# Kernel optimization log

Hardware: AMD Instinct MI355X
Metric: run time of the kernel (lower is better)

The kernel has to match this reference:

```python
import jax, jax.numpy as jnp
import numpy as np

EL = 512
B = 64
MASK_RAD = 20.0
EPS_SOFT = 0.25  # soft_equality epsilon


def soft_equality(x, value, epsilon):
    return jnp.exp(-((x - value) ** 2) / (2.0 * epsilon ** 2))


def two_point_autocorr(imgs):
    # imgs: (B, el, el). H=2 phases, but iA=iB=0 so only phase 0 contributes.
    el = imgs.shape[-1]
    mf0 = soft_equality(imgs, 0.0, EPS_SOFT)                 # (B, el, el)
    F = jnp.fft.fftn(mf0, axes=(-2, -1))                     # batched 2D FFT
    # term1*term2 = |F| e^{-i ang} * |F| e^{+i ang} = |F|^2 (iA == iB == 0)
    power = (F.real ** 2 + F.imag ** 2) / (el * el)
    ac = jnp.fft.ifftn(power.astype(jnp.complex64), axes=(-2, -1)).real
    # fft_shift: circular roll by half the image in both spatial dims
    return jnp.roll(ac, (el // 2, el // 2), axis=(-2, -1))


def batch_normalize(x):
    # per-image min-max normalization over all pixels
    b = x.shape[0]
    flat = x.reshape(b, -1)
    mn = jnp.min(flat, axis=1, keepdims=True)
    mx = jnp.max(flat, axis=1, keepdims=True)
    out = (flat - mn) / (mx - mn + 1e-12)
    return out.reshape(x.shape)


def gaussian_mask(rad, size):
    y = jnp.arange(size, dtype=jnp.float32)[:, None]
    x = jnp.arange(size, dtype=jnp.float32)[None, :]
    c = size // 2
    d2 = (x - c) ** 2 + (y - c) ** 2
    return jnp.exp(-d2 / (2.0 * rad ** 2))


def setup_inputs() -> dict:
    key = jax.random.key(0)
    k1, k2 = jax.random.split(key)
    inp = jax.random.uniform(k1, (B, 1, EL, EL), dtype=jnp.float32)
    tgt = jax.random.uniform(k2, (B, 1, EL, EL), dtype=jnp.float32)
    return {"input": inp, "target": tgt}


def reference(input, target):
    mask = gaussian_mask(MASK_RAD, EL)  # filtered=True
    ia = batch_normalize(two_point_autocorr(input[:, 0]))[:, None]   # (B,1,el,el)
    ta = batch_normalize(two_point_autocorr(target[:, 0]))[:, None]
    ia = ia * mask
    ta = ta * mask
    diff = jnp.mean((ia - ta) ** 2)
    input_and_ac = jnp.concatenate([input, ia], axis=3)
    target_and_ac = jnp.concatenate([target, ta], axis=3)
    return diff, input_and_ac, target_and_ac
```

## Files before the change

### kernel.cpp

```cpp
#include <hip/hip_runtime.h>

#define EL 512
#define NB 64
#define IMG (EL*EL)
#define HC 256

__device__ __forceinline__ void sb(){ __builtin_amdgcn_sched_barrier(0); }

__device__ __forceinline__ float2 cadd(float2 a, float2 b){ return make_float2(a.x+b.x, a.y+b.y); }
__device__ __forceinline__ float2 csub(float2 a, float2 b){ return make_float2(a.x-b.x, a.y-b.y); }
__device__ __forceinline__ float2 cmul(float2 a, float2 b){ return make_float2(a.x*b.x - a.y*b.y, a.x*b.y + a.y*b.x); }

template<int SIGN> __device__ __forceinline__ float2 mulW4(float2 a);
template<> __device__ __forceinline__ float2 mulW4<-1>(float2 a){ return make_float2( a.y, -a.x); }
template<> __device__ __forceinline__ float2 mulW4< 1>(float2 a){ return make_float2(-a.y,  a.x); }

template<int SIGN>
__device__ __forceinline__ void dft8(const float2* x, float2* X){
  float2 s04=cadd(x[0],x[4]), d04=csub(x[0],x[4]);
  float2 s26=cadd(x[2],x[6]), d26=csub(x[2],x[6]);
  float2 s15=cadd(x[1],x[5]), d15=csub(x[1],x[5]);
  float2 s37=cadd(x[3],x[7]), d37=csub(x[3],x[7]);
  float2 wd26 = mulW4<SIGN>(d26);
  float2 wd37 = mulW4<SIGN>(d37);
  float2 E0=cadd(s04,s26), E2=csub(s04,s26), E1=cadd(d04,wd26), E3=csub(d04,wd26);
  float2 O0=cadd(s15,s37), O2=csub(s15,s37), O1=cadd(d15,wd37), O3=csub(d15,wd37);
  const float C=0.70710678118654752440f;
  float2 w1 = make_float2(C, SIGN*C);
  float2 w3 = make_float2(-C, SIGN*C);
  float2 a1 = cmul(w1, O1);
  float2 a2 = mulW4<SIGN>(O2);
  float2 a3 = cmul(w3, O3);
  X[0]=cadd(E0,O0); X[4]=csub(E0,O0);
  X[1]=cadd(E1,a1); X[5]=csub(E1,a1);
  X[2]=cadd(E2,a2); X[6]=csub(E2,a2);
  X[3]=cadd(E3,a3); X[7]=csub(E3,a3);
}

__device__ __forceinline__ void twiddle8(float2 y[8], float cs, float sn){
  float2 w1 = make_float2(cs, sn);
  float2 w2 = cmul(w1, w1);
  float2 w3 = cmul(w2, w1);
  float2 w4 = cmul(w2, w2);
  float2 w5 = cmul(w4, w1);
  float2 w6 = cmul(w4, w2);
  float2 w7 = cmul(w4, w3);
  y[1] = cmul(y[1], w1);
  y[2] = cmul(y[2], w2);
  y[3] = cmul(y[3], w3);
  y[4] = cmul(y[4], w4);
  y[5] = cmul(y[5], w5);
  y[6] = cmul(y[6], w6);
  y[7] = cmul(y[7], w7);
}

template<int SIGN>
__device__ void fft512(float2 v[8], float2* buf, int lane){
  const float SGN = (float)SIGN;
  float sn, cs;
  float2 y[8];
  dft8<SIGN>(v, y);
  __sincosf(SGN * 0.012271846303085130f * (float)lane, &sn, &cs);
  twiddle8(y, cs, sn);
  sb();
  #pragma unroll
  for (int r=0;r<8;++r) buf[72*r + lane] = y[r];
  sb();
  int k0 = lane >> 3, n0 = lane & 7;
  float2 g[8];
  #pragma unroll
  for (int n1=0;n1<8;++n1) g[n1] = buf[72*k0 + 8*n1 + n0];
  float2 h[8];
  dft8<SIGN>(g, h);
  __sincosf(SGN * 0.098174770424681039f * (float)n0, &sn, &cs);
  twiddle8(h, cs, sn);
  sb();
  #pragma unroll
  for (int r=0;r<8;++r) buf[72*n0 + 9*k0 + r] = h[r];
  sb();
  int k0r = lane & 7, k1r = lane >> 3;
  float2 g2[8];
  #pragma unroll
  for (int m=0;m<8;++m) g2[m] = buf[72*m + 9*k0r + k1r];
  dft8<SIGN>(g2, v);
}

__device__ __forceinline__ unsigned fenc(float f){
  unsigned u = __float_as_uint(f);
  return (u & 0x80000000u) ? ~u : (u | 0x80000000u);
}
__device__ __forceinline__ float fdec(unsigned e){
  return (e & 0x80000000u) ? __uint_as_float(e & 0x7FFFFFFFu) : __uint_as_float(~e);
}

__global__ void k_init(double* accum, unsigned* umin, unsigned* umax){
  int t = threadIdx.x;
  if (t == 0) *accum = 0.0;
  if (t < 2*NB){ umin[t] = 0xFFFFFFFFu; umax[t] = 0u; }
}

__global__ __launch_bounds__(256)
void k_row_fwd(const float* __restrict__ in0, const float* __restrict__ in1,
               float2* __restrict__ cplx, float* __restrict__ outp,
               int base, int Pc){
  __shared__ float2 xbuf[4][576];
  int wave = threadIdx.x >> 6, lane = threadIdx.x & 63;
  int g = blockIdx.x >> 4;
  int rowblk = blockIdx.x & 15;
  bool isin = (g < Pc);
  int b = base + (isin ? g : g - Pc);
  const float* src = (isin ? in0 : in1) + (size_t)b * IMG;
  float* outhalf = outp + (isin ? (size_t)0 : (size_t)NB*EL*1024) + (size_t)b * EL * 1024;
  float2* S = cplx + (size_t)g * (IMG/2);
  float2* buf = xbuf[wave];
  for (int i=0;i<4;++i){
    int j = rowblk*16 + wave*4 + i;
    int y1 = 2*j, y2 = 2*j + 1;
    const float* s1 = src + (size_t)y1*EL;
    const float* s2 = src + (size_t)y2*EL;
    float2 v[8];
    #pragma unroll
    for (int a=0;a<8;++a){
      float x1 = s1[64*a + lane];
      float x2 = s2[64*a + lane];
      outhalf[(size_t)y1*1024 + 64*a + lane] = x1;
      outhalf[(size_t)y2*1024 + 64*a + lane] = x2;
      v[a] = make_float2(__expf(-8.0f*x1*x1), __expf(-8.0f*x2*x2));
    }
    fft512<-1>(v, buf, lane);
    sb();
    #pragma unroll
    for (int a=0;a<8;++a) buf[64*a + lane] = v[a];
    sb();
    float2 f1[4], f2[4];
    #pragma unroll
    for (int a=0;a<4;++a){
      float2 m = buf[(512 - (64*a + lane)) & 511];
      f1[a] = make_float2(0.5f*(v[a].x + m.x), 0.5f*(v[a].y - m.y));
      f2[a] = make_float2(0.5f*(v[a].y + m.y), 0.5f*(m.x - v[a].x));
    }
    if (lane == 0){
      float2 znyq = buf[256];
      f1[0] = make_float2(v[0].x, znyq.x);
      f2[0] = make_float2(v[0].y, znyq.y);
    }
    float2* S1 = S + (size_t)y1*HC;
    float2* S2 = S + (size_t)y2*HC;
    #pragma unroll
    for (int a=0;a<4;++a){
      S1[64*a + lane] = f1[a];
      S2[64*a + lane] = f2[a];
    }
  }
}

__global__ __launch_bounds__(256)
void k_col(float2* __restrict__ cplx){
  __shared__ float2 tile[8*580];
  int l = threadIdx.x;
  int wave = l >> 6, lane = l & 63;
  int g = blockIdx.x >> 5;
  int t = blockIdx.x & 31;
  int c0 = t*8;
  float2* S = cplx + (size_t)g*(IMG/2);
  {
    int cp = l & 3;
    int rb = l >> 2;
    for (int it=0; it<8; ++it){
      int r = rb + it*64;
      float4 v = *(const float4*)(S + (size_t)r*HC + c0 + 2*cp);
      tile[(2*cp+0)*580 + r] = make_float2(v.x, v.y);
      tile[(2*cp+1)*580 + r] = make_float2(v.z, v.w);
    }
  }
  __syncthreads();
  for (int cc=0; cc<2; ++cc){
    int c = wave*2 + cc;
    float2* slot = &tile[c*580];
    float2 v[8];
    #pragma unroll
    for (int a=0;a<8;++a) v[a] = slot[64*a + lane];
    fft512<-1>(v, slot, lane);
    if (c0 + c == 0){
      sb();
      #pragma unroll
      for (int a=0;a<8;++a) slot[64*a + lane] = v[a];
      sb();
      #pragma unroll
      for (int a=0;a<8;++a){
        float2 m = slot[(512 - (64*a + lane)) & 511];
        float2 g0 = make_float2(0.5f*(v[a].x + m.x), 0.5f*(v[a].y - m.y));
        float2 gn = make_float2(0.5f*(v[a].y + m.y), 0.5f*(m.x - v[a].x));
        v[a] = make_float2(g0.x*g0.x + g0.y*g0.y, gn.x*gn.x + gn.y*gn.y);
      }
      sb();
    } else {
      #pragma unroll
      for (int a=0;a<8;++a)
        v[a] = make_float2(v[a].x*v[a].x + v[a].y*v[a].y, 0.f);
    }
    fft512<1>(v, slot, lane);
    sb();
    #pragma unroll
    for (int a=0;a<8;++a) slot[64*a + lane] = v[a];
  }
  __syncthreads();
  {
    int cp = l & 3;
    int rb = l >> 2;
    for (int it=0; it<8; ++it){
      int r = rb + it*64;
      float2 e0 = tile[(2*cp+0)*580 + r];
      float2 e1 = tile[(2*cp+1)*580 + r];
      *(float4*)(S + (size_t)r*HC + c0 + 2*cp) = make_float4(e0.x, e0.y, e1.x, e1.y);
    }
  }
}

__global__ __launch_bounds__(256)
void k_row_inv(float2* __restrict__ cplx,
               unsigned* __restrict__ umin, unsigned* __restrict__ umax,
               int base, int Pc){
  __shared__ float2 xbuf[4][576];
  __shared__ float redmn[4], redmx[4];
  int wave = threadIdx.x >> 6, lane = threadIdx.x & 63;
  int g = blockIdx.x >> 4;
  int pblk = blockIdx.x & 15;
  float2* S = cplx + (size_t)g*(IMG/2);
  float* acb = (float*)S;
  float2* buf = xbuf[wave];
  const float SCALE = 1.0f / 68719476736.0f;
  float mn = 3.4e38f, mx = -3.4e38f;
  for (int i=0;i<4;++i){
    int p = pblk*16 + wave*4 + i;
    int y1 = p;
    int y2 = (p == 0) ? 256 : 512 - p;
    const float2* S1 = S + (size_t)y1*HC;
    const float2* S2 = S + (size_t)y2*HC;
    #pragma unroll
    for (int a=0;a<4;++a){
      buf[64*a + lane]       = S1[64*a + lane];
      buf[256 + 64*a + lane] = S2[64*a + lane];
    }
    sb();
    float2 v[8];
    #pragma unroll
    for (int a=0;a<8;++a){
      int kx = 64*a + lane;
      if (a < 4){
        float2 q1 = buf[kx], q2 = buf[256 + kx];
        v[a] = make_float2(q1.x - q2.y, q1.y + q2.x);
      } else {
        int kxp = (512 - kx) & 511;
        float2 q1 = buf[kxp], q2 = buf[256 + kxp];
        v[a] = make_float2(q1.x + q2.y, q2.x - q1.y);
      }
    }
    if (lane == 0){
      float2 A = buf[0], B = buf[256];
      bool self = (y1 == 0);
      float2 PA = self ? A : B;
      float2 PB = self ? B : A;
      float2 q0a = make_float2(0.5f*(A.x + PA.x), 0.5f*(A.y - PA.y));
      float2 qna = make_float2(0.5f*(A.y + PA.y), 0.5f*(PA.x - A.x));
      float2 q0b = make_float2(0.5f*(B.x + PB.x), 0.5f*(B.y - PB.y));
      float2 qnb = make_float2(0.5f*(B.y + PB.y), 0.5f*(PB.x - B.x));
      v[0] = make_float2(q0a.x - q0b.y, q0a.y + q0b.x);
      v[4] = make_float2(qna.x - qnb.y, qna.y + qnb.x);
    }
    sb();
    fft512<1>(v, buf, lane);
    float* d1 = acb + (size_t)y1*EL;
    float* d2 = acb + (size_t)y2*EL;
    #pragma unroll
    for (int a=0;a<8;++a){
      float a1 = v[a].x * SCALE;
      float a2 = v[a].y * SCALE;
      mn = fminf(mn, fminf(a1, a2)); mx = fmaxf(mx, fmaxf(a1, a2));
      d1[64*a + lane] = a1;
      d2[64*a + lane] = a2;
    }
  }
  for (int off=32; off>0; off>>=1){
    mn = fminf(mn, __shfl_down(mn, off, 64));
    mx = fmaxf(mx, __shfl_down(mx, off, 64));
  }
  if (lane==0){ redmn[wave]=mn; redmx[wave]=mx; }
  __syncthreads();
  if (threadIdx.x==0){
    mn = fminf(fminf(redmn[0],redmn[1]), fminf(redmn[2],redmn[3]));
    mx = fmaxf(fmaxf(redmx[0],redmx[1]), fmaxf(redmx[2],redmx[3]));
    int gid = (g < Pc) ? (base + g) : (NB + base + g - Pc);
    atomicMin(&umin[gid], fenc(mn));
    atomicMax(&umax[gid], fenc(mx));
  }
}

__global__ __launch_bounds__(256)
void k_final(const float2* __restrict__ cplx, const unsigned* __restrict__ umin,
             const unsigned* __restrict__ umax, float* __restrict__ outp,
             double* __restrict__ accum, int base, int Pc){
  __shared__ float red[4];
  int g    = blockIdx.x >> 5;
  int part = blockIdx.x & 31;
  int b = base + g;
  float mni = fdec(umin[b]),      mxi = fdec(umax[b]);
  float mnt = fdec(umin[NB + b]), mxt = fdec(umax[NB + b]);
  float inv_i = 1.0f / (mxi - mni + 1e-12f);
  float inv_t = 1.0f / (mxt - mnt + 1e-12f);
  const float* ai_b = (const float*)(cplx + (size_t)g * (IMG/2));
  const float* at_b = (const float*)(cplx + (size_t)(Pc + g) * (IMG/2));
  float* o_i = outp;
  float* o_t = outp + (size_t)NB * 512 * 1024;
  float acc = 0.f;
  for (int it=0; it<8; ++it){
    int q = it*256 + threadIdx.x;
    int y = part*16 + (q >> 7);
    int x = (q & 127) * 4;
    int sy = (y + 256) & 511, sx = (x + 256) & 511;
    float4 ai = *(const float4*)(ai_b + (size_t)sy*EL + sx);
    float4 at = *(const float4*)(at_b + (size_t)sy*EL + sx);
    float dy = (float)(y - 256); float dy2 = dy*dy;
    float dx0 = (float)(x - 256);
    float m0 = __expf(-((dx0+0)*(dx0+0) + dy2) * 0.00125f);
    float m1 = __expf(-((dx0+1)*(dx0+1) + dy2) * 0.00125f);
    float m2 = __expf(-((dx0+2)*(dx0+2) + dy2) * 0.00125f);
    float m3 = __expf(-((dx0+3)*(dx0+3) + dy2) * 0.00125f);
    float4 oi, ot;
    oi.x = (ai.x - mni)*inv_i*m0; ot.x = (at.x - mnt)*inv_t*m0;
    oi.y = (ai.y - mni)*inv_i*m1; ot.y = (at.y - mnt)*inv_t*m1;
    oi.z = (ai.z - mni)*inv_i*m2; ot.z = (at.z - mnt)*inv_t*m2;
    oi.w = (ai.w - mni)*inv_i*m3; ot.w = (at.w - mnt)*inv_t*m3;
    size_t rowo = ((size_t)b * 512 + (size_t)y) * 1024 + 512 + x;
    *(float4*)(o_i + 1 + rowo) = oi;
    *(float4*)(o_t + 1 + rowo) = ot;
    float d0 = oi.x - ot.x, d1 = oi.y - ot.y, d2 = oi.z - ot.z, d3 = oi.w - ot.w;
    acc += d0*d0 + d1*d1 + d2*d2 + d3*d3;
  }
  for (int off=32; off>0; off>>=1) acc += __shfl_down(acc, off, 64);
  int wave = threadIdx.x>>6, lane = threadIdx.x&63;
  if (lane==0) red[wave]=acc;
  __syncthreads();
  if (threadIdx.x==0) atomicAdd(accum, (double)(red[0]+red[1]+red[2]+red[3]));
}

__global__ void k_div(const double* accum, float* out0){
  out0[0] = (float)(*accum / 16777216.0);
}

extern "C" void kernel_launch(void* const* d_in, const int* in_sizes, int n_in,
                              void* d_out, int out_size, void* d_ws, size_t ws_size,
                              hipStream_t stream){
  (void)in_sizes; (void)n_in; (void)out_size;
  const float* in0 = (const float*)d_in[0];
  const float* in1 = (const float*)d_in[1];
  float* out = (float*)d_out;
  char* ws = (char*)d_ws;
  double*   accum = (double*)ws;
  unsigned* umin  = (unsigned*)(ws + 512);
  unsigned* umax  = (unsigned*)(ws + 1024);
  float2*   cplx  = (float2*)(ws + 4096);

  size_t avail = ws_size > 4096 ? ws_size - 4096 : 0;
  int P = (int)(avail / (2ull * 1024ull * 1024ull));
  if (P > NB) P = NB;
  if (P < 1)  P = 1;

  k_init<<<dim3(1), dim3(128), 0, stream>>>(accum, umin, umax);
  float* out1 = out + 1;
  for (int base = 0; base < NB; base += P){
    int Pc = (NB - base < P) ? (NB - base) : P;
    k_row_fwd<<<dim3(2*Pc*16), dim3(256), 0, stream>>>(in0, in1, cplx, out1, base, Pc);
    k_col    <<<dim3(2*Pc*32), dim3(256), 0, stream>>>(cplx);
    k_row_inv<<<dim3(2*Pc*16), dim3(256), 0, stream>>>(cplx, umin, umax, base, Pc);
    k_final  <<<dim3(Pc*32),   dim3(256), 0, stream>>>(cplx, umin, umax, out, accum, base, Pc);
  }
  k_div<<<dim3(1), dim3(1), 0, stream>>>(accum, out);
}
```

Before: 555.2 us.

## Use output buffer's autocorr half as FFT scratch and fold shift into spectrum

The half-spectrum intermediate is no longer kept in a separate workspace. It now lives in the right half of each output row, so the batch-chunked loop disappears and every kernel is launched once over all images. The fftshift roll is replaced by multiplying the spectrum by (-1)^k in both the column and inverse row passes. This lets k_final read and write in place without the strided shifted gather. Output rows are 1024 floats apart (offset by one element), so the float4 accesses may be misaligned and the strided layout may cost some coalescing.

```diff
diff --git a/kernel.cpp b/kernel.cpp
--- a/kernel.cpp
+++ b/kernel.cpp
@@ -3,7 +3,8 @@
 #define EL 512
 #define NB 64
 #define IMG (EL*EL)
-#define HC 256
+#define ROWF 1024
+#define IMGF (EL*ROWF)
 
 __device__ __forceinline__ void sb(){ __builtin_amdgcn_sched_barrier(0); }
 
@@ -101,30 +102,30 @@
 
 __global__ __launch_bounds__(256)
 void k_row_fwd(const float* __restrict__ in0, const float* __restrict__ in1,
-               float2* __restrict__ cplx, float* __restrict__ outp,
-               int base, int Pc){
+               float* __restrict__ out1){
   __shared__ float2 xbuf[4][576];
   int wave = threadIdx.x >> 6, lane = threadIdx.x & 63;
   int g = blockIdx.x >> 4;
   int rowblk = blockIdx.x & 15;
-  bool isin = (g < Pc);
-  int b = base + (isin ? g : g - Pc);
+  bool isin = (g < NB);
+  int b = isin ? g : g - NB;
   const float* src = (isin ? in0 : in1) + (size_t)b * IMG;
-  float* outhalf = outp + (isin ? (size_t)0 : (size_t)NB*EL*1024) + (size_t)b * EL * 1024;
-  float2* S = cplx + (size_t)g * (IMG/2);
+  float* obase = out1 + (isin ? (size_t)0 : (size_t)NB*IMGF) + (size_t)b * IMGF;
   float2* buf = xbuf[wave];
   for (int i=0;i<4;++i){
     int j = rowblk*16 + wave*4 + i;
     int y1 = 2*j, y2 = 2*j + 1;
     const float* s1 = src + (size_t)y1*EL;
     const float* s2 = src + (size_t)y2*EL;
+    float* o1 = obase + (size_t)y1*ROWF;
+    float* o2 = obase + (size_t)y2*ROWF;
     float2 v[8];
     #pragma unroll
     for (int a=0;a<8;++a){
       float x1 = s1[64*a + lane];
       float x2 = s2[64*a + lane];
-      outhalf[(size_t)y1*1024 + 64*a + lane] = x1;
-      outhalf[(size_t)y2*1024 + 64*a + lane] = x2;
+      o1[64*a + lane] = x1;
+      o2[64*a + lane] = x2;
       v[a] = make_float2(__expf(-8.0f*x1*x1), __expf(-8.0f*x2*x2));
     }
     fft512<-1>(v, buf, lane);
@@ -144,8 +145,8 @@
       f1[0] = make_float2(v[0].x, znyq.x);
       f2[0] = make_float2(v[0].y, znyq.y);
     }
-    float2* S1 = S + (size_t)y1*HC;
-    float2* S2 = S + (size_t)y2*HC;
+    float2* S1 = (float2*)(o1 + EL);
+    float2* S2 = (float2*)(o2 + EL);
     #pragma unroll
     for (int a=0;a<4;++a){
       S1[64*a + lane] = f1[a];
@@ -155,25 +156,28 @@
 }
 
 __global__ __launch_bounds__(256)
-void k_col(float2* __restrict__ cplx){
+void k_col(float* __restrict__ out1){
   __shared__ float2 tile[8*580];
   int l = threadIdx.x;
   int wave = l >> 6, lane = l & 63;
   int g = blockIdx.x >> 5;
   int t = blockIdx.x & 31;
   int c0 = t*8;
-  float2* S = cplx + (size_t)g*(IMG/2);
+  bool isin = (g < NB);
+  int b = isin ? g : g - NB;
+  float* sbase = out1 + (isin ? (size_t)0 : (size_t)NB*IMGF) + (size_t)b*IMGF + EL;
   {
     int cp = l & 3;
     int rb = l >> 2;
     for (int it=0; it<8; ++it){
       int r = rb + it*64;
-      float4 v = *(const float4*)(S + (size_t)r*HC + c0 + 2*cp);
+      float4 v = *(const float4*)(sbase + (size_t)r*ROWF + 2*(c0 + 2*cp));
       tile[(2*cp+0)*580 + r] = make_float2(v.x, v.y);
       tile[(2*cp+1)*580 + r] = make_float2(v.z, v.w);
     }
   }
   __syncthreads();
+  float sgn = (lane & 1) ? -1.f : 1.f;
   for (int cc=0; cc<2; ++cc){
     int c = wave*2 + cc;
     float2* slot = &tile[c*580];
@@ -191,13 +195,14 @@
         float2 m = slot[(512 - (64*a + lane)) & 511];
         float2 g0 = make_float2(0.5f*(v[a].x + m.x), 0.5f*(v[a].y - m.y));
         float2 gn = make_float2(0.5f*(v[a].y + m.y), 0.5f*(m.x - v[a].x));
-        v[a] = make_float2(g0.x*g0.x + g0.y*g0.y, gn.x*gn.x + gn.y*gn.y);
+        v[a] = make_float2(sgn*(g0.x*g0.x + g0.y*g0.y),
+                           sgn*(gn.x*gn.x + gn.y*gn.y));
       }
       sb();
     } else {
       #pragma unroll
       for (int a=0;a<8;++a)
-        v[a] = make_float2(v[a].x*v[a].x + v[a].y*v[a].y, 0.f);
+        v[a] = make_float2(sgn*(v[a].x*v[a].x + v[a].y*v[a].y), 0.f);
     }
     fft512<1>(v, slot, lane);
     sb();
@@ -212,31 +217,32 @@
       int r = rb + it*64;
       float2 e0 = tile[(2*cp+0)*580 + r];
       float2 e1 = tile[(2*cp+1)*580 + r];
-      *(float4*)(S + (size_t)r*HC + c0 + 2*cp) = make_float4(e0.x, e0.y, e1.x, e1.y);
+      *(float4*)(sbase + (size_t)r*ROWF + 2*(c0 + 2*cp)) = make_float4(e0.x, e0.y, e1.x, e1.y);
     }
   }
 }
 
 __global__ __launch_bounds__(256)
-void k_row_inv(float2* __restrict__ cplx,
-               unsigned* __restrict__ umin, unsigned* __restrict__ umax,
-               int base, int Pc){
+void k_row_inv(float* __restrict__ out1,
+               unsigned* __restrict__ umin, unsigned* __restrict__ umax){
   __shared__ float2 xbuf[4][576];
   __shared__ float redmn[4], redmx[4];
   int wave = threadIdx.x >> 6, lane = threadIdx.x & 63;
   int g = blockIdx.x >> 4;
   int pblk = blockIdx.x & 15;
-  float2* S = cplx + (size_t)g*(IMG/2);
-  float* acb = (float*)S;
+  bool isin = (g < NB);
+  int b = isin ? g : g - NB;
+  float* sbase = out1 + (isin ? (size_t)0 : (size_t)NB*IMGF) + (size_t)b*IMGF + EL;
   float2* buf = xbuf[wave];
   const float SCALE = 1.0f / 68719476736.0f;
+  float sgn = (lane & 1) ? -1.f : 1.f;
   float mn = 3.4e38f, mx = -3.4e38f;
   for (int i=0;i<4;++i){
     int p = pblk*16 + wave*4 + i;
     int y1 = p;
     int y2 = (p == 0) ? 256 : 512 - p;
-    const float2* S1 = S + (size_t)y1*HC;
-    const float2* S2 = S + (size_t)y2*HC;
+    const float2* S1 = (const float2*)(sbase + (size_t)y1*ROWF);
+    const float2* S2 = (const float2*)(sbase + (size_t)y2*ROWF);
     #pragma unroll
     for (int a=0;a<4;++a){
       buf[64*a + lane]       = S1[64*a + lane];
@@ -268,10 +274,12 @@
       v[0] = make_float2(q0a.x - q0b.y, q0a.y + q0b.x);
       v[4] = make_float2(qna.x - qnb.y, qna.y + qnb.x);
     }
+    #pragma unroll
+    for (int a=0;a<8;++a){ v[a].x *= sgn; v[a].y *= sgn; }
     sb();
     fft512<1>(v, buf, lane);
-    float* d1 = acb + (size_t)y1*EL;
-    float* d2 = acb + (size_t)y2*EL;
+    float* d1 = sbase + (size_t)y1*ROWF;
+    float* d2 = sbase + (size_t)y2*ROWF;
     #pragma unroll
     for (int a=0;a<8;++a){
       float a1 = v[a].x * SCALE;
@@ -290,36 +298,33 @@
   if (threadIdx.x==0){
     mn = fminf(fminf(redmn[0],redmn[1]), fminf(redmn[2],redmn[3]));
     mx = fmaxf(fmaxf(redmx[0],redmx[1]), fmaxf(redmx[2],redmx[3]));
-    int gid = (g < Pc) ? (base + g) : (NB + base + g - Pc);
+    int gid = isin ? b : (NB + b);
     atomicMin(&umin[gid], fenc(mn));
     atomicMax(&umax[gid], fenc(mx));
   }
 }
 
 __global__ __launch_bounds__(256)
-void k_final(const float2* __restrict__ cplx, const unsigned* __restrict__ umin,
-             const unsigned* __restrict__ umax, float* __restrict__ outp,
-             double* __restrict__ accum, int base, int Pc){
+void k_final(float* __restrict__ out1, const unsigned* __restrict__ umin,
+             const unsigned* __restrict__ umax, double* __restrict__ accum){
   __shared__ float red[4];
-  int g    = blockIdx.x >> 5;
+  int b    = blockIdx.x >> 5;
   int part = blockIdx.x & 31;
-  int b = base + g;
   float mni = fdec(umin[b]),      mxi = fdec(umax[b]);
   float mnt = fdec(umin[NB + b]), mxt = fdec(umax[NB + b]);
   float inv_i = 1.0f / (mxi - mni + 1e-12f);
   float inv_t = 1.0f / (mxt - mnt + 1e-12f);
-  const float* ai_b = (const float*)(cplx + (size_t)g * (IMG/2));
-  const float* at_b = (const float*)(cplx + (size_t)(Pc + g) * (IMG/2));
-  float* o_i = outp;
-  float* o_t = outp + (size_t)NB * 512 * 1024;
+  float* ai_b = out1 + (size_t)b*IMGF + EL;
+  float* at_b = ai_b + (size_t)NB*IMGF;
   float acc = 0.f;
   for (int it=0; it<8; ++it){
     int q = it*256 + threadIdx.x;
     int y = part*16 + (q >> 7);
     int x = (q & 127) * 4;
-    int sy = (y + 256) & 511, sx = (x + 256) & 511;
-    float4 ai = *(const float4*)(ai_b + (size_t)sy*EL + sx);
-    float4 at = *(const float4*)(at_b + (size_t)sy*EL + sx);
+    float* pi = ai_b + (size_t)y*ROWF + x;
+    float* pt = at_b + (size_t)y*ROWF + x;
+    float4 ai = *(const float4*)pi;
+    float4 at = *(const float4*)pt;
     float dy = (float)(y - 256); float dy2 = dy*dy;
     float dx0 = (float)(x - 256);
     float m0 = __expf(-((dx0+0)*(dx0+0) + dy2) * 0.00125f);
@@ -331,9 +336,8 @@
     oi.y = (ai.y - mni)*inv_i*m1; ot.y = (at.y - mnt)*inv_t*m1;
     oi.z = (ai.z - mni)*inv_i*m2; ot.z = (at.z - mnt)*inv_t*m2;
     oi.w = (ai.w - mni)*inv_i*m3; ot.w = (at.w - mnt)*inv_t*m3;
-    size_t rowo = ((size_t)b * 512 + (size_t)y) * 1024 + 512 + x;
-    *(float4*)(o_i + 1 + rowo) = oi;
-    *(float4*)(o_t + 1 + rowo) = ot;
+    *(float4*)pi = oi;
+    *(float4*)pt = ot;
     float d0 = oi.x - ot.x, d1 = oi.y - ot.y, d2 = oi.z - ot.z, d3 = oi.w - ot.w;
     acc += d0*d0 + d1*d1 + d2*d2 + d3*d3;
   }
@@ -351,7 +355,7 @@
 extern "C" void kernel_launch(void* const* d_in, const int* in_sizes, int n_in,
                               void* d_out, int out_size, void* d_ws, size_t ws_size,
                               hipStream_t stream){
-  (void)in_sizes; (void)n_in; (void)out_size;
+  (void)in_sizes; (void)n_in; (void)out_size; (void)ws_size;
   const float* in0 = (const float*)d_in[0];
   const float* in1 = (const float*)d_in[1];
   float* out = (float*)d_out;
@@ -359,21 +363,12 @@
   double*   accum = (double*)ws;
   unsigned* umin  = (unsigned*)(ws + 512);
   unsigned* umax  = (unsigned*)(ws + 1024);
-  float2*   cplx  = (float2*)(ws + 4096);
-
-  size_t avail = ws_size > 4096 ? ws_size - 4096 : 0;
-  int P = (int)(avail / (2ull * 1024ull * 1024ull));
-  if (P > NB) P = NB;
-  if (P < 1)  P = 1;
-
-  k_init<<<dim3(1), dim3(128), 0, stream>>>(accum, umin, umax);
   float* out1 = out + 1;
-  for (int base = 0; base < NB; base += P){
-    int Pc = (NB - base < P) ? (NB - base) : P;
-    k_row_fwd<<<dim3(2*Pc*16), dim3(256), 0, stream>>>(in0, in1, cplx, out1, base, Pc);
-    k_col    <<<dim3(2*Pc*32), dim3(256), 0, stream>>>(cplx);
-    k_row_inv<<<dim3(2*Pc*16), dim3(256), 0, stream>>>(cplx, umin, umax, base, Pc);
-    k_final  <<<dim3(Pc*32),   dim3(256), 0, stream>>>(cplx, umin, umax, out, accum, base, Pc);
-  }
-  k_div<<<dim3(1), dim3(1), 0, stream>>>(accum, out);
-}
+
+  k_init   <<<dim3(1),        dim3(128), 0, stream>>>(accum, umin, umax);
+  k_row_fwd<<<dim3(2*NB*16),  dim3(256), 0, stream>>>(in0, in1, out1);
+  k_col    <<<dim3(2*NB*32),  dim3(256), 0, stream>>>(out1);
+  k_row_inv<<<dim3(2*NB*16),  dim3(256), 0, stream>>>(out1, umin, umax);
+  k_final  <<<dim3(NB*32),    dim3(256), 0, stream>>>(out1, umin, umax, accum);
+  k_div    <<<dim3(1),        dim3(1),   0, stream>>>(accum, out);
+}
```

After: 611.7 us. 1.1x slower.
